# Performance work log

Hardware: AMD Instinct MI355X
Metric: run time of the kernel (lower is better)

Reference implementation:

```python
import jax, jax.numpy as jnp
import numpy as np

G = 4            # group order (e.g., C4)
H = 16           # attention heads
DH = 64          # head dim
D = 1024         # token dim = H*DH = C*G
DI = 4096        # FFN inner dim
MAXREL = 32      # relative position clamp
EPS = 1e-5


def eq_ln(x):
    # Equivariant LayerNorm: (N, D) -> (N, G, D/G), LN over last dim, no affine
    N, Dt = x.shape
    xr = x.reshape(N, G, Dt // G)
    mu = jnp.mean(xr, axis=-1, keepdims=True)
    var = jnp.var(xr, axis=-1, keepdims=True)
    return ((xr - mu) * jax.lax.rsqrt(var + EPS)).reshape(N, Dt)


def ada_ln(x, temb, w, b):
    # AdaLN: scale/shift from SiLU(temb) -> Linear -> chunk
    n = eq_ln(x)
    ss = jax.nn.silu(temb) @ w.T + b                      # (N, 2D)
    scale, shift = jnp.split(ss, 2, axis=1)
    return n * (1.0 + scale) + shift


def attention(xq, xkv, wq, wk, wv, wo, bo, rel_table):
    # xq: (B,Tq,D), xkv: (B,Tk,D); rel_table: (H, 2*MAXREL+1) or None
    B, Tq, _ = xq.shape
    Tk = xkv.shape[1]
    q = (xq @ wq.T).reshape(B, Tq, H, DH)
    k = (xkv @ wk.T).reshape(B, Tk, H, DH)
    v = (xkv @ wv.T).reshape(B, Tk, H, DH)
    scores = jnp.einsum('bthd,bkhd->bhtk', q, k) * (DH ** -0.5)
    if rel_table is not None:
        rel_idx = jnp.clip(jnp.arange(Tq)[:, None] - jnp.arange(Tk)[None, :],
                           -MAXREL, MAXREL) + MAXREL      # (Tq, Tk)
        scores = scores + rel_table[:, rel_idx][None]     # (1,H,Tq,Tk)
    attn = jax.nn.softmax(scores, axis=-1)
    out = jnp.einsum('bhtk,bkhd->bthd', attn, v).reshape(B, Tq, H * DH)
    return out @ wo.T + bo


def setup_inputs() -> dict:
    key = jax.random.key(0)
    ks = jax.random.split(key, 24)
    s = 0.02
    B, T = 4, 1024
    inp = {
        'hidden_states': jax.random.normal(ks[0], (B, T, D), jnp.float32),
        'encoder_hidden_states': jax.random.normal(ks[1], (B, T, D), jnp.float32),
        'temb': jax.random.normal(ks[2], (B * T, D), jnp.float32),
        # AdaLN 1 / 2
        'w_ada1': jax.random.normal(ks[3], (2 * D, D), jnp.float32) * s,
        'b_ada1': jnp.zeros((2 * D,), jnp.float32),
        'w_ada2': jax.random.normal(ks[4], (2 * D, D), jnp.float32) * s,
        'b_ada2': jnp.zeros((2 * D,), jnp.float32),
        # self-attention (attention_bias=False, out_bias=True)
        'wq1': jax.random.normal(ks[5], (D, D), jnp.float32) * s,
        'wk1': jax.random.normal(ks[6], (D, D), jnp.float32) * s,
        'wv1': jax.random.normal(ks[7], (D, D), jnp.float32) * s,
        'wo1': jax.random.normal(ks[8], (D, D), jnp.float32) * s,
        'bo1': jnp.zeros((D,), jnp.float32),
        'rel_bias': jax.random.normal(ks[9], (H, 2 * MAXREL + 1), jnp.float32) * s,
        # cross-attention
        'wq2': jax.random.normal(ks[10], (D, D), jnp.float32) * s,
        'wk2': jax.random.normal(ks[11], (D, D), jnp.float32) * s,
        'wv2': jax.random.normal(ks[12], (D, D), jnp.float32) * s,
        'wo2': jax.random.normal(ks[13], (D, D), jnp.float32) * s,
        'bo2': jnp.zeros((D,), jnp.float32),
        # GEGLU FFN
        'w_ff1': jax.random.normal(ks[14], (2 * DI, D), jnp.float32) * s,
        'b_ff1': jnp.zeros((2 * DI,), jnp.float32),
        'w_ff2': jax.random.normal(ks[15], (D, DI), jnp.float32) * s,
        'b_ff2': jnp.zeros((D,), jnp.float32),
    }
    return inp


def reference(hidden_states, encoder_hidden_states, temb,
              w_ada1, b_ada1, w_ada2, b_ada2,
              wq1, wk1, wv1, wo1, bo1, rel_bias,
              wq2, wk2, wv2, wo2, bo2,
              w_ff1, b_ff1, w_ff2, b_ff2):
    B, T, Dm = hidden_states.shape
    x = hidden_states.reshape(B * T, Dm)
    # 1) AdaLN + self-attention with relative position bias + residual
    x1 = ada_ln(x, temb, w_ada1, b_ada1).reshape(B, T, Dm)
    x = x + attention(x1, x1, wq1, wk1, wv1, wo1, bo1, rel_bias).reshape(B * T, Dm)
    # 2) AdaLN + cross-attention + residual
    x2 = ada_ln(x, temb, w_ada2, b_ada2).reshape(B, T, Dm)
    x = x + attention(x2, encoder_hidden_states, wq2, wk2, wv2, wo2, bo2,
                      None).reshape(B * T, Dm)
    # 3) LayerNorm + GEGLU FFN + residual
    n3 = eq_ln(x)
    h12 = n3 @ w_ff1.T + b_ff1                            # (N, 2*DI)
    a, g = jnp.split(h12, 2, axis=-1)
    ff = (a * jax.nn.gelu(g, approximate=False)) @ w_ff2.T + b_ff2
    x = x + ff
    return x.reshape(B, T, Dm)
```

## Files before the change

kernel.cpp:

```cpp
#include <hip/hip_runtime.h>
#include <math.h>

typedef __attribute__((ext_vector_type(4))) float f32x4;
typedef __attribute__((ext_vector_type(8))) __bf16 bf16x8;

#define MFMA_BF16(a, b, c) __builtin_amdgcn_mfma_f32_16x16x32_bf16((a), (b), (c), 0, 0, 0)

static __device__ __forceinline__ unsigned short f2b(float f) {
  unsigned int u = __float_as_uint(f);
  return (unsigned short)((u + 0x7FFFu + ((u >> 16) & 1u)) >> 16);
}
static __device__ __forceinline__ float b2f(unsigned short h) {
  return __uint_as_float(((unsigned int)h) << 16);
}
static __device__ __forceinline__ unsigned short bcvt(float f) {
  __bf16 h = (__bf16)f;
  return __builtin_bit_cast(unsigned short, h);
}

static __device__ __forceinline__ void gll16(const void* g, void* l) {
  __builtin_amdgcn_global_load_lds((const __attribute__((address_space(1))) void*)g,
                                   (__attribute__((address_space(3))) void*)l, 16, 0, 0);
}

struct CvtArgs {
  const float* src[12];
  unsigned short* dst[12];
  int start[12];
};
__global__ __launch_bounds__(256) void f2b_multi(CvtArgs a) {
  const int bid = blockIdx.x;
  int s = 11;
#pragma unroll
  for (int i = 11; i >= 1; --i)
    if (bid < a.start[i]) s = i - 1;
  const size_t i4 = (size_t)(bid - a.start[s]) * 256 + threadIdx.x;
  const float4 v = *(const float4*)(a.src[s] + i4 * 4);
  ushort4 o;
  o.x = f2b(v.x); o.y = f2b(v.y); o.z = f2b(v.z); o.w = f2b(v.w);
  *(ushort4*)(a.dst[s] + i4 * 4) = o;
}

__global__ __launch_bounds__(256) void f2bperm_kernel(const float* __restrict__ src,
                                                      unsigned short* __restrict__ dst) {
  const int r = blockIdx.x;
  const int rr = r & 4095;
  const int dr = ((rr >> 4) << 5) | ((r >> 12) << 4) | (rr & 15);
  const int c = threadIdx.x * 4;
  const float4 v = *(const float4*)(src + (size_t)r * 1024 + c);
  ushort4 o;
  o.x = f2b(v.x); o.y = f2b(v.y); o.z = f2b(v.z); o.w = f2b(v.w);
  *(ushort4*)(dst + (size_t)dr * 1024 + c) = o;
}

__global__ __launch_bounds__(256) void silu_kernel(const float* __restrict__ src,
                                                   unsigned short* __restrict__ dst, int n) {
  const int i = (blockIdx.x * 256 + threadIdx.x) * 4;
  if (i >= n) return;
  const float4 v = *(const float4*)(src + i);
  ushort4 o;
  o.x = f2b(v.x / (1.f + expf(-v.x)));
  o.y = f2b(v.y / (1.f + expf(-v.y)));
  o.z = f2b(v.z / (1.f + expf(-v.z)));
  o.w = f2b(v.w / (1.f + expf(-v.w)));
  *(ushort4*)(dst + i) = o;
}

template <int ADA>
__global__ __launch_bounds__(256) void eqln_kernel(const float* __restrict__ x,
                                                   const unsigned short* __restrict__ ss,
                                                   unsigned short* __restrict__ outp) {
  const int n = blockIdx.x;
  const int tid = threadIdx.x;
  const int g = tid >> 6, lane = tid & 63;
  const size_t base = (size_t)n * 1024 + g * 256 + lane * 4;
  const float4 v = *(const float4*)(x + base);
  float s = v.x + v.y + v.z + v.w;
  float s2 = v.x * v.x + v.y * v.y + v.z * v.z + v.w * v.w;
#pragma unroll
  for (int m = 1; m < 64; m <<= 1) {
    s += __shfl_xor(s, m, 64);
    s2 += __shfl_xor(s2, m, 64);
  }
  const float mu = s * (1.f / 256.f);
  const float var = s2 * (1.f / 256.f) - mu * mu;
  const float rs = rsqrtf(var + 1e-5f);
  float o0 = (v.x - mu) * rs, o1 = (v.y - mu) * rs, o2 = (v.z - mu) * rs, o3 = (v.w - mu) * rs;
  if (ADA) {
    const size_t sb = (size_t)n * 4096 + g * 256 + lane * 4;
    const ushort4 scv = *(const ushort4*)(ss + sb);
    const ushort4 shv = *(const ushort4*)(ss + sb + 1024);
    o0 = o0 * (1.f + b2f(scv.x)) + b2f(shv.x);
    o1 = o1 * (1.f + b2f(scv.y)) + b2f(shv.y);
    o2 = o2 * (1.f + b2f(scv.z)) + b2f(shv.z);
    o3 = o3 * (1.f + b2f(scv.w)) + b2f(shv.w);
  }
  ushort4 ov;
  ov.x = f2b(o0); ov.y = f2b(o1); ov.z = f2b(o2); ov.w = f2b(o3);
  *(ushort4*)(outp + base) = ov;
}

__global__ __launch_bounds__(256) void vtrans_kernel(const unsigned short* __restrict__ v,
                                                     unsigned short* __restrict__ vt, int T,
                                                     int ld) {
  const int t0 = blockIdx.x * 64, h = blockIdx.y, b = blockIdx.z;
  __shared__ unsigned short tile[64][65];
  const int tid = threadIdx.x;
#pragma unroll
  for (int rr = 0; rr < 2; ++rr) {
    const int tok = rr * 32 + (tid >> 3);
    const int d8 = (tid & 7) * 8;
    const uint4 x = *(const uint4*)(v + (size_t)(b * T + t0 + tok) * ld + h * 64 + d8);
    const unsigned int* xs = (const unsigned int*)&x;
#pragma unroll
    for (int j = 0; j < 4; ++j) {
      tile[d8 + 2 * j][tok] = (unsigned short)(xs[j] & 0xffffu);
      tile[d8 + 2 * j + 1][tok] = (unsigned short)(xs[j] >> 16);
    }
  }
  __syncthreads();
#pragma unroll
  for (int rr = 0; rr < 2; ++rr) {
    const int d = rr * 32 + (tid >> 3);
    const int t8 = (tid & 7) * 8;
    uint4 ov;
    unsigned int* ou = (unsigned int*)&ov;
#pragma unroll
    for (int j = 0; j < 4; ++j)
      ou[j] = (unsigned int)tile[d][t8 + 2 * j] | ((unsigned int)tile[d][t8 + 2 * j + 1] << 16);
    *(uint4*)(vt + ((size_t)((b * 16 + h) * 64 + d)) * T + t0 + t8) = ov;
  }
}

template <int BM, int BIAS, int RES, int OUTMODE>
__global__ __launch_bounds__(256, 4) void gemm_nt(const unsigned short* __restrict__ A,
                                                  const unsigned short* __restrict__ Bw,
                                                  const float* __restrict__ bias,
                                                  const float* res, void* Cout,
                                                  int M, int N, int K) {
  constexpr int MB = BM / 32;
  __shared__ unsigned short As[BM * 64];
  __shared__ unsigned short Bs[128 * 64];
  const int m0 = blockIdx.x * BM, n0 = blockIdx.y * 128;
  const int tid = threadIdx.x, lane = tid & 63;
  const int wr = (tid >> 7) & 1, wc = (tid >> 6) & 1;
  const int lr = lane & 15, ls = lane >> 4;

  const f32x4 fz = {0.f, 0.f, 0.f, 0.f};
  f32x4 acc[MB][4];
#pragma unroll
  for (int m = 0; m < MB; ++m)
#pragma unroll
    for (int n = 0; n < 4; ++n) acc[m][n] = fz;

  for (int k0 = 0; k0 < K; k0 += 64) {
#pragma unroll
    for (int it = 0; it < BM / 32; ++it) {
      const int u = it * 256 + tid;
      const int row = u >> 3, gs = (u & 7) ^ (row & 7);
      gll16(A + (size_t)(m0 + row) * K + k0 + gs * 8, As + u * 8);
    }
#pragma unroll
    for (int it = 0; it < 4; ++it) {
      const int u = it * 256 + tid;
      const int row = u >> 3, gs = (u & 7) ^ (row & 7);
      gll16(Bw + (size_t)(n0 + row) * K + k0 + gs * 8, Bs + u * 8);
    }
    __syncthreads();
#pragma unroll
    for (int kk = 0; kk < 2; ++kk) {
      bf16x8 af[MB], bfr[4];
#pragma unroll
      for (int m = 0; m < MB; ++m) {
        const int row = wr * (BM / 2) + m * 16 + lr;
        const int slot = (kk * 4 + ls) ^ (row & 7);
        af[m] = *(const bf16x8*)(As + row * 64 + slot * 8);
      }
#pragma unroll
      for (int n = 0; n < 4; ++n) {
        const int col = wc * 64 + n * 16 + lr;
        const int slot = (kk * 4 + ls) ^ (col & 7);
        bfr[n] = *(const bf16x8*)(Bs + col * 64 + slot * 8);
      }
#pragma unroll
      for (int m = 0; m < MB; ++m)
#pragma unroll
        for (int n = 0; n < 4; ++n) acc[m][n] = MFMA_BF16(af[m], bfr[n], acc[m][n]);
    }
    __syncthreads();
  }

  if (OUTMODE == 2) {
    const int pn0 = n0 + wc * 64;
#pragma unroll
    for (int m = 0; m < MB; ++m) {
#pragma unroll
      for (int j = 0; j < 2; ++j) {
        const int ocol = (pn0 >> 1) + j * 16 + lr;
        const float ba = bias[ocol];
        const float bg = bias[(N >> 1) + ocol];
#pragma unroll
        for (int r = 0; r < 4; ++r) {
          const int row = m0 + wr * (BM / 2) + m * 16 + ls * 4 + r;
          const float a = acc[m][2 * j][r] + ba;
          const float g = acc[m][2 * j + 1][r] + bg;
          const float gl = 0.5f * g * (1.f + erff(g * 0.70710678118654752f));
          ((unsigned short*)Cout)[(size_t)row * (N >> 1) + ocol] = f2b(a * gl);
        }
      }
    }
    return;
  }
#pragma unroll
  for (int m = 0; m < MB; ++m) {
#pragma unroll
    for (int n = 0; n < 4; ++n) {
      const int col = n0 + wc * 64 + n * 16 + lr;
      float bv = 0.f;
      if (BIAS) bv = bias[col];
#pragma unroll
      for (int r = 0; r < 4; ++r) {
        const int row = m0 + wr * (BM / 2) + m * 16 + ls * 4 + r;
        float v = acc[m][n][r] + bv;
        if (RES) v += res[(size_t)row * N + col];
        if (OUTMODE == 1)
          ((unsigned short*)Cout)[(size_t)row * N + col] = f2b(v);
        else
          ((float*)Cout)[(size_t)row * N + col] = v;
      }
    }
  }
}

template <int RELB>
__global__ __launch_bounds__(256) void attn_kernel(const unsigned short* __restrict__ q,
                                                   const unsigned short* __restrict__ k,
                                                   const unsigned short* __restrict__ vt,
                                                   const float* __restrict__ rel,
                                                   unsigned short* __restrict__ outp,
                                                   int ldq, int ldk) {
  const int lin = blockIdx.x + (blockIdx.y << 4) + (blockIdx.z << 8);
  const int xcd = lin & 7, s = lin >> 3;
  const int g = (xcd << 3) + (s >> 4);
  const int qb = s & 15;
  const int h = g & 15, b = g >> 4;
  const int tid = threadIdx.x;
  const int wid = tid >> 6, lane = tid & 63;
  const int lr = lane & 15, ls = lane >> 4;
  const int q0 = (qb << 6) + (wid << 4);
  const float L2E = 1.44269504088896340736f;

  __shared__ unsigned short Ks[2][128 * 64];
  __shared__ unsigned short plds[4][16][64];
  __shared__ float tbl[66];

  if (RELB && tid < 65) tbl[tid] = rel[h * 65 + tid] * L2E;

  bf16x8 qa0, qa1;
  {
    const unsigned short* qp = q + (size_t)(b * 1024 + q0 + lr) * ldq + h * 64 + ls * 8;
    const bf16x8 t0 = *(const bf16x8*)qp;
    const bf16x8 t1 = *(const bf16x8*)(qp + 32);
    const float sc = 0.125f * L2E;
#pragma unroll
    for (int j = 0; j < 8; ++j) {
      qa0[j] = (__bf16)((float)t0[j] * sc);
      qa1[j] = (__bf16)((float)t1[j] * sc);
    }
  }
  bf16x8 ones;
#pragma unroll
  for (int j = 0; j < 8; ++j) ones[j] = (__bf16)1.0f;

  const f32x4 fz = {0.f, 0.f, 0.f, 0.f};
  f32x4 oacc[4];
#pragma unroll
  for (int d = 0; d < 4; ++d) oacc[d] = fz;
  f32x4 lacc = fz;

  const unsigned short* kbp = k + (size_t)(b * 1024) * ldk + h * 64;
  const unsigned short* vbp = vt + (size_t)((b * 16 + h) * 64) * 1024;

#pragma unroll
  for (int it = 0; it < 4; ++it) {
    const int u = it * 256 + tid;
    const int row = u >> 3, gs = (u & 7) ^ (row & 7);
    gll16(kbp + (size_t)row * ldk + gs * 8, Ks[0] + u * 8);
  }
  __syncthreads();

  for (int t = 0; t < 8; ++t) {
    const int kv0 = t << 7;
    bf16x8 vr[16];
#pragma unroll
    for (int hf = 0; hf < 2; ++hf)
#pragma unroll
      for (int d = 0; d < 4; ++d) {
        const unsigned short* vp = vbp + (size_t)(d * 16 + lr) * 1024 + kv0 + hf * 64 + ls * 8;
        vr[hf * 8 + 2 * d] = *(const bf16x8*)vp;
        vr[hf * 8 + 2 * d + 1] = *(const bf16x8*)(vp + 32);
      }
    if (t + 1 < 8) {
      const unsigned short* kst = kbp + (size_t)((t + 1) << 7) * ldk;
#pragma unroll
      for (int it = 0; it < 4; ++it) {
        const int u = it * 256 + tid;
        const int row = u >> 3, gs = (u & 7) ^ (row & 7);
        gll16(kst + (size_t)row * ldk + gs * 8, Ks[(t + 1) & 1] + u * 8);
      }
    }
    const unsigned short* kbuf = Ks[t & 1];
#pragma unroll
    for (int sub = 0; sub < 2; ++sub) {
      const int kvs = kv0 + sub * 64;
      f32x4 sc4[4];
      __builtin_amdgcn_s_setprio(1);
#pragma unroll
      for (int nn = 0; nn < 4; ++nn) {
        const int row = sub * 64 + nn * 16 + lr;
        const int s0 = ls ^ (row & 7), s1 = (4 + ls) ^ (row & 7);
        const bf16x8 kb0 = *(const bf16x8*)(kbuf + row * 64 + s0 * 8);
        const bf16x8 kb1 = *(const bf16x8*)(kbuf + row * 64 + s1 * 8);
        f32x4 acc = fz;
        acc = MFMA_BF16(qa0, kb0, acc);
        acc = MFMA_BF16(qa1, kb1, acc);
        sc4[nn] = acc;
      }
      __builtin_amdgcn_s_setprio(0);
      float cb = 0.f;
      bool vary = false;
      if (RELB) {
        if (kvs + 95 <= q0) {
          cb = tbl[64];
        } else if (kvs >= q0 + 47) {
          cb = tbl[0];
        } else {
          vary = true;
        }
      }
      if (vary) {
        const int bd = q0 + ls * 4 - (kvs + lr);
#pragma unroll
        for (int nn = 0; nn < 4; ++nn)
#pragma unroll
          for (int r = 0; r < 4; ++r) {
            int dl = bd + r - nn * 16;
            dl = dl < -32 ? -32 : (dl > 32 ? 32 : dl);
            const float p = __builtin_amdgcn_exp2f(fminf(sc4[nn][r] + tbl[dl + 32], 60.f));
            const int qq = ls * 4 + r;
            const int colw = ((((nn << 1) + (lr >> 3)) ^ (qq & 7)) << 3) + (lr & 7);
            plds[wid][qq][colw] = bcvt(p);
          }
      } else {
#pragma unroll
        for (int nn = 0; nn < 4; ++nn)
#pragma unroll
          for (int r = 0; r < 4; ++r) {
            const float p = __builtin_amdgcn_exp2f(fminf(sc4[nn][r] + cb, 60.f));
            const int qq = ls * 4 + r;
            const int colw = ((((nn << 1) + (lr >> 3)) ^ (qq & 7)) << 3) + (lr & 7);
            plds[wid][qq][colw] = bcvt(p);
          }
      }
      asm volatile("" ::: "memory");
      const bf16x8 pa0 = *(const bf16x8*)&plds[wid][lr][((ls ^ (lr & 7)) << 3)];
      const bf16x8 pa1 = *(const bf16x8*)&plds[wid][lr][(((4 + ls) ^ (lr & 7)) << 3)];
      __builtin_amdgcn_s_setprio(1);
      lacc = MFMA_BF16(pa0, ones, lacc);
      lacc = MFMA_BF16(pa1, ones, lacc);
#pragma unroll
      for (int d = 0; d < 4; ++d) {
        oacc[d] = MFMA_BF16(pa0, vr[sub * 8 + 2 * d], oacc[d]);
        oacc[d] = MFMA_BF16(pa1, vr[sub * 8 + 2 * d + 1], oacc[d]);
      }
      __builtin_amdgcn_s_setprio(0);
    }
    __syncthreads();
  }

  float rinv[4];
#pragma unroll
  for (int r = 0; r < 4; ++r) rinv[r] = 1.0f / lacc[r];
#pragma unroll
  for (int d = 0; d < 4; ++d)
#pragma unroll
    for (int r = 0; r < 4; ++r) {
      const float v = oacc[d][r] * rinv[r];
      outp[(size_t)(b * 1024 + q0 + ls * 4 + r) * 1024 + h * 64 + d * 16 + lr] = bcvt(v);
    }
}

extern "C" void kernel_launch(void* const* d_in, const int* in_sizes, int n_in,
                              void* d_out, int out_size, void* d_ws, size_t ws_size,
                              hipStream_t stream) {
  (void)in_sizes; (void)n_in; (void)out_size; (void)ws_size;
  const float* hs = (const float*)d_in[0];
  const float* enc = (const float*)d_in[1];
  const float* temb = (const float*)d_in[2];
  const float* wada1 = (const float*)d_in[3];
  const float* bada1 = (const float*)d_in[4];
  const float* wada2 = (const float*)d_in[5];
  const float* bada2 = (const float*)d_in[6];
  const float* wq1 = (const float*)d_in[7];
  const float* wk1 = (const float*)d_in[8];
  const float* wv1 = (const float*)d_in[9];
  const float* wo1 = (const float*)d_in[10];
  const float* bo1 = (const float*)d_in[11];
  const float* rel = (const float*)d_in[12];
  const float* wq2 = (const float*)d_in[13];
  const float* wk2 = (const float*)d_in[14];
  const float* wv2 = (const float*)d_in[15];
  const float* wo2 = (const float*)d_in[16];
  const float* bo2 = (const float*)d_in[17];
  const float* wff1 = (const float*)d_in[18];
  const float* bff1 = (const float*)d_in[19];
  const float* wff2 = (const float*)d_in[20];
  const float* bff2 = (const float*)d_in[21];
  float* out = (float*)d_out;

  char* ws = (char*)d_ws;
  const size_t MB = 1024ull * 1024ull;
  unsigned short* wb_ada = (unsigned short*)(ws + 0 * MB);
  unsigned short* wb_q1 = (unsigned short*)(ws + 8 * MB);
  unsigned short* wb_k1 = (unsigned short*)(ws + 10 * MB);
  unsigned short* wb_v1 = (unsigned short*)(ws + 12 * MB);
  unsigned short* wb_o1 = (unsigned short*)(ws + 14 * MB);
  unsigned short* wb_q2 = (unsigned short*)(ws + 16 * MB);
  unsigned short* wb_k2 = (unsigned short*)(ws + 18 * MB);
  unsigned short* wb_v2 = (unsigned short*)(ws + 20 * MB);
  unsigned short* wb_o2 = (unsigned short*)(ws + 22 * MB);
  unsigned short* wb_ff1 = (unsigned short*)(ws + 24 * MB);
  unsigned short* wb_ff2 = (unsigned short*)(ws + 40 * MB);
  unsigned short* silu_t = (unsigned short*)(ws + 48 * MB);
  unsigned short* enc_b = (unsigned short*)(ws + 56 * MB);
  unsigned short* ssb = (unsigned short*)(ws + 64 * MB);
  unsigned short* ffin = (unsigned short*)(ws + 64 * MB);
  float* bias_cat = (float*)(ws + 96 * MB);
  unsigned short* x1b = (unsigned short*)(ws + 97 * MB);
  unsigned short* qkvb = (unsigned short*)(ws + 105 * MB);
  unsigned short* qb = (unsigned short*)(ws + 105 * MB);
  unsigned short* kvb = (unsigned short*)(ws + 113 * MB);
  unsigned short* vtb = (unsigned short*)(ws + 129 * MB);
  unsigned short* aob = (unsigned short*)(ws + 137 * MB);

  const int Nrow = 4096;

  {
    CvtArgs a;
    const float* srcs[12] = {wada1, wada2, wq1, wk1, wv1, wo1, wq2, wk2, wv2, wo2, wff2, enc};
    unsigned short* dsts[12] = {wb_ada, wb_ada + 2048 * 1024, wb_q1, wb_k1, wb_v1, wb_o1,
                                wb_q2, wb_k2, wb_v2, wb_o2, wb_ff2, enc_b};
    const int blks[12] = {2048, 2048, 1024, 1024, 1024, 1024, 1024, 1024, 1024, 1024, 4096, 4096};
    int acc = 0;
    for (int i = 0; i < 12; ++i) { a.src[i] = srcs[i]; a.dst[i] = dsts[i]; a.start[i] = acc; acc += blks[i]; }
    f2b_multi<<<acc, 256, 0, stream>>>(a);
  }
  (void)hipMemcpyAsync(bias_cat, bada1, 2048 * sizeof(float), hipMemcpyDeviceToDevice, stream);
  (void)hipMemcpyAsync(bias_cat + 2048, bada2, 2048 * sizeof(float), hipMemcpyDeviceToDevice, stream);
  f2bperm_kernel<<<8192, 256, 0, stream>>>(wff1, wb_ff1);
  silu_kernel<<<4096, 256, 0, stream>>>(temb, silu_t, 4096 * 1024);

  gemm_nt<128, 1, 0, 1><<<dim3(32, 32), 256, 0, stream>>>(silu_t, wb_ada, bias_cat, nullptr, ssb, Nrow, 4096, 1024);

  eqln_kernel<1><<<4096, 256, 0, stream>>>(hs, ssb, x1b);
  gemm_nt<128, 0, 0, 1><<<dim3(32, 24), 256, 0, stream>>>(x1b, wb_q1, nullptr, nullptr, qkvb, Nrow, 3072, 1024);
  vtrans_kernel<<<dim3(16, 16, 4), 256, 0, stream>>>(qkvb + 2048, vtb, 1024, 3072);
  attn_kernel<1><<<dim3(16, 16, 4), 256, 0, stream>>>(qkvb, qkvb + 1024, vtb, rel, aob, 3072, 3072);
  gemm_nt<64, 1, 1, 0><<<dim3(64, 8), 256, 0, stream>>>(aob, wb_o1, bo1, hs, out, Nrow, 1024, 1024);

  eqln_kernel<1><<<4096, 256, 0, stream>>>(out, ssb + 2048, x1b);
  gemm_nt<64, 0, 0, 1><<<dim3(64, 8), 256, 0, stream>>>(x1b, wb_q2, nullptr, nullptr, qb, Nrow, 1024, 1024);
  gemm_nt<128, 0, 0, 1><<<dim3(32, 16), 256, 0, stream>>>(enc_b, wb_k2, nullptr, nullptr, kvb, Nrow, 2048, 1024);
  vtrans_kernel<<<dim3(16, 16, 4), 256, 0, stream>>>(kvb + 1024, vtb, 1024, 2048);
  attn_kernel<0><<<dim3(16, 16, 4), 256, 0, stream>>>(qb, kvb, vtb, nullptr, aob, 1024, 2048);
  gemm_nt<64, 1, 1, 0><<<dim3(64, 8), 256, 0, stream>>>(aob, wb_o2, bo2, out, out, Nrow, 1024, 1024);

  eqln_kernel<0><<<4096, 256, 0, stream>>>(out, nullptr, x1b);
  gemm_nt<128, 1, 0, 2><<<dim3(32, 64), 256, 0, stream>>>(x1b, wb_ff1, bff1, nullptr, ffin, Nrow, 8192, 1024);
  gemm_nt<64, 1, 1, 0><<<dim3(64, 8), 256, 0, stream>>>(ffin, wb_ff2, bff2, out, out, Nrow, 1024, 4096);
}
```

Baseline: 486.4 us.

## Load attention K tiles directly into registers with ping-pong prefetch, drop LDS staging

The attention kernel no longer stages K blocks through a double-buffered shared-memory tile with block-wide barriers. Each wave now loads its K fragments for 64-key tiles straight from global memory into registers, prefetching the next tile into an alternate register set. This removes per-tile __syncthreads and LDS traffic for K, but every wave now fetches K separately (4x more global/L2 reads) and register pressure rises.

```diff
diff --git a/kernel.cpp b/kernel.cpp
--- a/kernel.cpp
+++ b/kernel.cpp
@@ -230,6 +230,89 @@
       }
     }
   }
+}
+
+template <int RELB>
+static __device__ __forceinline__ void attn_tile_v7(
+    int kv0, bool pre, const unsigned short* __restrict__ kbp, int ldk,
+    const unsigned short* __restrict__ vbp,
+    const bf16x8& qa0, const bf16x8& qa1, const bf16x8& ones,
+    bf16x8 (&kc)[8], bf16x8 (&kn)[8],
+    f32x4 (&oacc)[4], f32x4& lacc,
+    const float* tbl, unsigned short (*pw)[64], int lr, int ls, int q0) {
+  const f32x4 fz = {0.f, 0.f, 0.f, 0.f};
+  bf16x8 vr[8];
+#pragma unroll
+  for (int d = 0; d < 4; ++d) {
+    const unsigned short* vp = vbp + (size_t)(d * 16 + lr) * 1024 + kv0 + ls * 8;
+    vr[2 * d] = *(const bf16x8*)vp;
+    vr[2 * d + 1] = *(const bf16x8*)(vp + 32);
+  }
+  if (pre) {
+#pragma unroll
+    for (int nn = 0; nn < 4; ++nn) {
+      const unsigned short* kp = kbp + (size_t)(kv0 + 64 + nn * 16 + lr) * ldk + ls * 8;
+      kn[2 * nn] = *(const bf16x8*)kp;
+      kn[2 * nn + 1] = *(const bf16x8*)(kp + 32);
+    }
+  }
+  f32x4 s[4];
+  __builtin_amdgcn_s_setprio(1);
+#pragma unroll
+  for (int nn = 0; nn < 4; ++nn) {
+    f32x4 t = fz;
+    t = MFMA_BF16(qa0, kc[2 * nn], t);
+    t = MFMA_BF16(qa1, kc[2 * nn + 1], t);
+    s[nn] = t;
+  }
+  __builtin_amdgcn_s_setprio(0);
+  float cb = 0.f;
+  bool vary = false;
+  if (RELB) {
+    if (kv0 + 95 <= q0) {
+      cb = tbl[64];
+    } else if (kv0 >= q0 + 47) {
+      cb = tbl[0];
+    } else {
+      vary = true;
+    }
+  }
+  if (vary) {
+    const int bd = q0 + ls * 4 - (kv0 + lr);
+#pragma unroll
+    for (int nn = 0; nn < 4; ++nn)
+#pragma unroll
+      for (int r = 0; r < 4; ++r) {
+        int dl = bd + r - nn * 16;
+        dl = dl < -32 ? -32 : (dl > 32 ? 32 : dl);
+        const float p = __builtin_amdgcn_exp2f(fminf(s[nn][r] + tbl[dl + 32], 60.f));
+        const int qq = ls * 4 + r;
+        const int colw = ((((nn << 1) + (lr >> 3)) ^ (qq & 7)) << 3) + (lr & 7);
+        pw[qq][colw] = bcvt(p);
+      }
+  } else {
+#pragma unroll
+    for (int nn = 0; nn < 4; ++nn)
+#pragma unroll
+      for (int r = 0; r < 4; ++r) {
+        const float p = __builtin_amdgcn_exp2f(fminf(s[nn][r] + cb, 60.f));
+        const int qq = ls * 4 + r;
+        const int colw = ((((nn << 1) + (lr >> 3)) ^ (qq & 7)) << 3) + (lr & 7);
+        pw[qq][colw] = bcvt(p);
+      }
+  }
+  asm volatile("" ::: "memory");
+  const bf16x8 pa0 = *(const bf16x8*)&pw[lr][((ls ^ (lr & 7)) << 3)];
+  const bf16x8 pa1 = *(const bf16x8*)&pw[lr][(((4 + ls) ^ (lr & 7)) << 3)];
+  __builtin_amdgcn_s_setprio(1);
+  lacc = MFMA_BF16(pa0, ones, lacc);
+  lacc = MFMA_BF16(pa1, ones, lacc);
+#pragma unroll
+  for (int d = 0; d < 4; ++d) {
+    oacc[d] = MFMA_BF16(pa0, vr[2 * d], oacc[d]);
+    oacc[d] = MFMA_BF16(pa1, vr[2 * d + 1], oacc[d]);
+  }
+  __builtin_amdgcn_s_setprio(0);
 }
 
 template <int RELB>
@@ -250,11 +333,13 @@
   const int q0 = (qb << 6) + (wid << 4);
   const float L2E = 1.44269504088896340736f;
 
-  __shared__ unsigned short Ks[2][128 * 64];
   __shared__ unsigned short plds[4][16][64];
   __shared__ float tbl[66];
 
-  if (RELB && tid < 65) tbl[tid] = rel[h * 65 + tid] * L2E;
+  if (RELB) {
+    if (tid < 65) tbl[tid] = rel[h * 65 + tid] * L2E;
+    __syncthreads();
+  }
 
   bf16x8 qa0, qa1;
   {
@@ -281,101 +366,20 @@
   const unsigned short* kbp = k + (size_t)(b * 1024) * ldk + h * 64;
   const unsigned short* vbp = vt + (size_t)((b * 16 + h) * 64) * 1024;
 
-#pragma unroll
-  for (int it = 0; it < 4; ++it) {
-    const int u = it * 256 + tid;
-    const int row = u >> 3, gs = (u & 7) ^ (row & 7);
-    gll16(kbp + (size_t)row * ldk + gs * 8, Ks[0] + u * 8);
-  }
-  __syncthreads();
-
-  for (int t = 0; t < 8; ++t) {
-    const int kv0 = t << 7;
-    bf16x8 vr[16];
-#pragma unroll
-    for (int hf = 0; hf < 2; ++hf)
-#pragma unroll
-      for (int d = 0; d < 4; ++d) {
-        const unsigned short* vp = vbp + (size_t)(d * 16 + lr) * 1024 + kv0 + hf * 64 + ls * 8;
-        vr[hf * 8 + 2 * d] = *(const bf16x8*)vp;
-        vr[hf * 8 + 2 * d + 1] = *(const bf16x8*)(vp + 32);
-      }
-    if (t + 1 < 8) {
-      const unsigned short* kst = kbp + (size_t)((t + 1) << 7) * ldk;
-#pragma unroll
-      for (int it = 0; it < 4; ++it) {
-        const int u = it * 256 + tid;
-        const int row = u >> 3, gs = (u & 7) ^ (row & 7);
-        gll16(kst + (size_t)row * ldk + gs * 8, Ks[(t + 1) & 1] + u * 8);
-      }
-    }
-    const unsigned short* kbuf = Ks[t & 1];
-#pragma unroll
-    for (int sub = 0; sub < 2; ++sub) {
-      const int kvs = kv0 + sub * 64;
-      f32x4 sc4[4];
-      __builtin_amdgcn_s_setprio(1);
-#pragma unroll
-      for (int nn = 0; nn < 4; ++nn) {
-        const int row = sub * 64 + nn * 16 + lr;
-        const int s0 = ls ^ (row & 7), s1 = (4 + ls) ^ (row & 7);
-        const bf16x8 kb0 = *(const bf16x8*)(kbuf + row * 64 + s0 * 8);
-        const bf16x8 kb1 = *(const bf16x8*)(kbuf + row * 64 + s1 * 8);
-        f32x4 acc = fz;
-        acc = MFMA_BF16(qa0, kb0, acc);
-        acc = MFMA_BF16(qa1, kb1, acc);
-        sc4[nn] = acc;
-      }
-      __builtin_amdgcn_s_setprio(0);
-      float cb = 0.f;
-      bool vary = false;
-      if (RELB) {
-        if (kvs + 95 <= q0) {
-          cb = tbl[64];
-        } else if (kvs >= q0 + 47) {
-          cb = tbl[0];
-        } else {
-          vary = true;
-        }
-      }
-      if (vary) {
-        const int bd = q0 + ls * 4 - (kvs + lr);
-#pragma unroll
-        for (int nn = 0; nn < 4; ++nn)
-#pragma unroll
-          for (int r = 0; r < 4; ++r) {
-            int dl = bd + r - nn * 16;
-            dl = dl < -32 ? -32 : (dl > 32 ? 32 : dl);
-            const float p = __builtin_amdgcn_exp2f(fminf(sc4[nn][r] + tbl[dl + 32], 60.f));
-            const int qq = ls * 4 + r;
-            const int colw = ((((nn << 1) + (lr >> 3)) ^ (qq & 7)) << 3) + (lr & 7);
-            plds[wid][qq][colw] = bcvt(p);
-          }
-      } else {
-#pragma unroll
-        for (int nn = 0; nn < 4; ++nn)
-#pragma unroll
-          for (int r = 0; r < 4; ++r) {
-            const float p = __builtin_amdgcn_exp2f(fminf(sc4[nn][r] + cb, 60.f));
-            const int qq = ls * 4 + r;
-            const int colw = ((((nn << 1) + (lr >> 3)) ^ (qq & 7)) << 3) + (lr & 7);
-            plds[wid][qq][colw] = bcvt(p);
-          }
-      }
-      asm volatile("" ::: "memory");
-      const bf16x8 pa0 = *(const bf16x8*)&plds[wid][lr][((ls ^ (lr & 7)) << 3)];
-      const bf16x8 pa1 = *(const bf16x8*)&plds[wid][lr][(((4 + ls) ^ (lr & 7)) << 3)];
-      __builtin_amdgcn_s_setprio(1);
-      lacc = MFMA_BF16(pa0, ones, lacc);
-      lacc = MFMA_BF16(pa1, ones, lacc);
-#pragma unroll
-      for (int d = 0; d < 4; ++d) {
-        oacc[d] = MFMA_BF16(pa0, vr[sub * 8 + 2 * d], oacc[d]);
-        oacc[d] = MFMA_BF16(pa1, vr[sub * 8 + 2 * d + 1], oacc[d]);
-      }
-      __builtin_amdgcn_s_setprio(0);
-    }
-    __syncthreads();
+  bf16x8 kA[8], kB[8];
+#pragma unroll
+  for (int nn = 0; nn < 4; ++nn) {
+    const unsigned short* kp = kbp + (size_t)(nn * 16 + lr) * ldk + ls * 8;
+    kA[2 * nn] = *(const bf16x8*)kp;
+    kA[2 * nn + 1] = *(const bf16x8*)(kp + 32);
+  }
+
+#pragma unroll 1
+  for (int t = 0; t < 16; t += 2) {
+    attn_tile_v7<RELB>(t << 6, true, kbp, ldk, vbp, qa0, qa1, ones, kA, kB,
+                       oacc, lacc, tbl, plds[wid], lr, ls, q0);
+    attn_tile_v7<RELB>((t + 1) << 6, t + 1 < 15, kbp, ldk, vbp, qa0, qa1, ones, kB, kA,
+                       oacc, lacc, tbl, plds[wid], lr, ls, q0);
   }
 
   float rinv[4];
```

After: 572.6 us. +17.7%, slower.
